# Kernel optimization log

Measured on AMD Instinct MI355X. Metric: run time of the kernel, lower is better.

Reference implementation:

```python
import jax, jax.numpy as jnp
import numpy as np

NUM_CATS = 8
ACTION_DIM = 64
HIDDEN = 1024  # out_type.size == config.hidden_size
N_TOKENS = 4096  # B*T
N_BATCH = 128    # timesteps batch; tiled to N_TOKENS in forward


def sinusoidal_pos_encoding(t, dim):
    # standard transformer sinusoidal encoding; t: (N,) -> (N, dim)
    half = dim // 2
    div = jnp.exp(jnp.arange(half, dtype=jnp.float32) * (-np.log(10000.0) / half))
    ang = t.astype(jnp.float32)[:, None] * div[None, :]          # (N, half)
    pe = jnp.stack([jnp.sin(ang), jnp.cos(ang)], axis=-1)        # (N, half, 2)
    return pe.reshape(t.shape[0], dim)


def cat_linear(x, W, b, cat_ids):
    """Per-category linear (gather -> per-group GEMM -> scatter-back, fused).
    x: (N, din), W: (C, din, dout), b: (C, dout), cat_ids: (N,) int.
    Mathematically identical to the torch loop over unique cat ids."""
    y_all = jnp.einsum('nd,cdo->nco', x, W)                      # dense dispatch over C
    y = jnp.take_along_axis(y_all, cat_ids[:, None, None], axis=1)[:, 0, :]
    return y + b[cat_ids]


def setup_inputs() -> dict:
    key = jax.random.key(0)
    ks = jax.random.split(key, 9)
    inp = {
        'actions': jax.random.normal(ks[0], (N_TOKENS, ACTION_DIM), dtype=jnp.float32),
        'timesteps': jax.random.randint(ks[1], (N_BATCH,), 0, 1000, dtype=jnp.int32),
        'cat_ids': jax.random.randint(ks[2], (N_TOKENS,), 0, NUM_CATS, dtype=jnp.int32),
        'W1': jax.random.normal(ks[3], (NUM_CATS, ACTION_DIM, HIDDEN), dtype=jnp.float32) / np.sqrt(ACTION_DIM),
        'b1': jax.random.normal(ks[4], (NUM_CATS, HIDDEN), dtype=jnp.float32) * 0.02,
        'W2': jax.random.normal(ks[5], (NUM_CATS, 2 * HIDDEN, HIDDEN), dtype=jnp.float32) / np.sqrt(2 * HIDDEN),
        'b2': jax.random.normal(ks[6], (NUM_CATS, HIDDEN), dtype=jnp.float32) * 0.02,
        'W3': jax.random.normal(ks[7], (NUM_CATS, HIDDEN, HIDDEN), dtype=jnp.float32) / np.sqrt(HIDDEN),
        'b3': jax.random.normal(ks[8], (NUM_CATS, HIDDEN), dtype=jnp.float32) * 0.02,
    }
    return inp


def reference(actions, timesteps, cat_ids, W1, b1, W2, b2, W3, b3):
    n = actions.shape[0]
    # timesteps.repeat(B // timesteps.shape[0]) in torch tiles the whole tensor
    t_full = jnp.tile(timesteps, n // timesteps.shape[0])        # (N,)
    a_emb = cat_linear(actions, W1, b1, cat_ids)                 # (N, H)
    tau_emb = sinusoidal_pos_encoding(t_full, HIDDEN).astype(a_emb.dtype)
    x = jnp.concatenate([a_emb, tau_emb], axis=-1)               # (N, 2H)
    x = jax.nn.silu(cat_linear(x, W2, b2, cat_ids))              # swish
    x = cat_linear(x, W3, b3, cat_ids)                           # (N, H)
    return x
```

## Files before the change

kernel.cpp:

```cpp
#include <hip/hip_runtime.h>
#include <cmath>


#define NTOK 4096
#define HID  1024
#define NC   8
#define MPAD 4224

typedef _Float16 f16;
typedef _Float16 f16x8 __attribute__((ext_vector_type(8)));
typedef float    f32x4 __attribute__((ext_vector_type(4)));

#define GLDS16(g, l) __builtin_amdgcn_global_load_lds(                      \
    (const __attribute__((address_space(1))) void*)(g),                     \
    (__attribute__((address_space(3))) void*)(l), 16, 0, 0)
#define WAITV(n) asm volatile("s_waitcnt vmcnt(" #n ")" ::: "memory")

__global__ void build_perm_kernel(const int* __restrict__ cat,
                                  int* __restrict__ perm,
                                  int* __restrict__ cat_off,
                                  int* __restrict__ tmap) {
  __shared__ int cnt[NC];
  __shared__ int off[NC + 1];
  const int tid = threadIdx.x;
  if (tid < NC) cnt[tid] = 0;
  __syncthreads();
  for (int n = tid; n < NTOK; n += blockDim.x) atomicAdd(&cnt[cat[n]], 1);
  __syncthreads();
  if (tid == 0) {
    int s = 0;
    for (int c = 0; c < NC; ++c) { off[c] = s; s += cnt[c]; }
    off[NC] = s;
    int ns = 0;
    for (int c = 0; c < NC; ++c) {
      const int n = off[c + 1] - off[c];
      for (int m0 = 0; m0 < n; m0 += 64) tmap[1 + ns++] = (c << 20) | m0;
    }
    tmap[0] = ns;
  }
  __syncthreads();
  if (tid < NC) cnt[tid] = off[tid];
  if (tid <= NC) cat_off[tid] = off[tid];
  __syncthreads();
  for (int n = tid; n < NTOK; n += blockDim.x) {
    int pos = atomicAdd(&cnt[cat[n]], 1);
    perm[pos] = n;
  }
}

__global__ void tau16_kernel(const int* __restrict__ ts, f16* __restrict__ tau) {
  const int b = blockIdx.x;
  const float t = (float)ts[b];
  const float cdiv = -0.017988946039015984f;
  for (int i = threadIdx.x; i < HID / 2; i += blockDim.x) {
    float ang = t * expf(cdiv * (float)i);
    tau[(size_t)b * HID + 2 * i]     = (f16)sinf(ang);
    tau[(size_t)b * HID + 2 * i + 1] = (f16)cosf(ang);
  }
}

__global__ void gather_kernel(const float* __restrict__ actions,
                              const f16* __restrict__ tau,
                              const int* __restrict__ perm,
                              f16* __restrict__ act_g, f16* __restrict__ xcat) {
  const int r = blockIdx.x;
  const int tok = perm[r];
  const int t = threadIdx.x;
  if (t < 64) act_g[(size_t)r * 64 + t] = (f16)actions[(size_t)tok * 64 + t];
  const uint4* src = (const uint4*)(tau + (size_t)(tok & 127) * HID);
  uint4* dst = (uint4*)(xcat + (size_t)r * 2048 + HID);
  dst[t] = src[t];
}

__global__ __launch_bounds__(256) void wcvt_kernel(const float* __restrict__ W,
                                                   f16* __restrict__ Wt, int K) {
  const int c = blockIdx.z, k0 = blockIdx.y * 64, n0 = blockIdx.x * 64;
  __shared__ f16 tl[64][68];
  const int tid = threadIdx.x;
  const int rr = tid >> 4, cs = (tid & 15) * 4;
  const float* src = W + ((size_t)c * K + k0) * HID + n0;
#pragma unroll
  for (int it = 0; it < 4; ++it) {
    const int kr = rr + it * 16;
    float4 v = *(const float4*)(src + (size_t)kr * HID + cs);
    tl[kr][cs + 0] = (f16)v.x;
    tl[kr][cs + 1] = (f16)v.y;
    tl[kr][cs + 2] = (f16)v.z;
    tl[kr][cs + 3] = (f16)v.w;
  }
  __syncthreads();
  f16* dst = Wt + ((size_t)c * HID + n0) * K + k0;
#pragma unroll
  for (int it = 0; it < 4; ++it) {
    const int nr = rr + it * 16;
    union { f16 h[4]; uint2 u; } pk;
    pk.h[0] = tl[cs + 0][nr];
    pk.h[1] = tl[cs + 1][nr];
    pk.h[2] = tl[cs + 2][nr];
    pk.h[3] = tl[cs + 3][nr];
    *(uint2*)(dst + (size_t)nr * K + cs) = pk.u;
  }
}

template <int K, int MODE>
__global__ __launch_bounds__(256, 2) void mfma_gemm(
    const f16* __restrict__ A, const f16* __restrict__ Wt,
    const float* __restrict__ Bias, const int* __restrict__ perm,
    const int* __restrict__ cat_off, const int* __restrict__ tmap,
    void* __restrict__ OutV) {
  constexpr int PA = (MODE == 0) ? 64 : (MODE == 1) ? 2048 : 1024;
  constexpr int BK = 64;
  constexpr int NT = K / BK;

  const int nslots = tmap[0];
  if ((int)blockIdx.y >= nslots) return;
  const int ent = tmap[1 + blockIdx.y];
  const int c = ent >> 20, m0 = ent & 0xFFF;
  const int g0 = cat_off[c], cnt = cat_off[c + 1] - g0;
  const int n0 = blockIdx.x * 128;

  __shared__ f16 As[3][64 * BK];
  __shared__ f16 Bs[3][128 * BK];
  __shared__ int rows[64];

  const int tid = threadIdx.x;
  const int lane = tid & 63, wid = tid >> 6;
  const int wm = wid >> 1, wn = wid & 1;
  const int fr = lane & 15, fq = lane >> 4;

  if (MODE == 2 && tid < 64) {
    int m = m0 + tid;
    if (m > cnt - 1) m = cnt - 1;
    rows[tid] = perm[g0 + m];
  }

  const f16* Abase = A + (size_t)(g0 + m0) * PA;
  const f16* Bbase = Wt + ((size_t)c * HID + n0) * K;

#define STAGE(buf, kt)                                                        \
  do {                                                                        \
    _Pragma("unroll") for (int i_ = 0; i_ < 2; ++i_) {                        \
      const int s_ = tid + i_ * 256;                                          \
      const int r_ = s_ >> 3, qg_ = (s_ & 7) ^ (r_ & 7);                      \
      GLDS16(Abase + (size_t)r_ * PA + (kt) + qg_ * 8, &As[buf][s_ * 8]);     \
    }                                                                         \
    _Pragma("unroll") for (int i_ = 0; i_ < 4; ++i_) {                        \
      const int s_ = tid + i_ * 256;                                          \
      const int r_ = s_ >> 3, qg_ = (s_ & 7) ^ (r_ & 7);                      \
      GLDS16(Bbase + (size_t)r_ * K + (kt) + qg_ * 8, &Bs[buf][s_ * 8]);      \
    }                                                                         \
  } while (0)

  f32x4 acc[2][4];
#pragma unroll
  for (int i = 0; i < 2; ++i)
#pragma unroll
    for (int j = 0; j < 4; ++j) acc[i][j] = (f32x4){0.f, 0.f, 0.f, 0.f};

  STAGE(0, 0);
  if (NT > 1) STAGE(1, BK);

  for (int t = 0; t < NT; ++t) {
    if (t + 1 < NT) { WAITV(6); } else { WAITV(0); }
    __builtin_amdgcn_s_barrier();
    const int cur = t % 3;

    f16x8 af[2][2], bf[2][4];
#pragma unroll
    for (int ks = 0; ks < 2; ++ks) {
      const int q = ks * 4 + fq;
#pragma unroll
      for (int i = 0; i < 2; ++i) {
        const int r = wm * 32 + i * 16 + fr;
        af[ks][i] = *(const f16x8*)&As[cur][r * 64 + ((q ^ (r & 7)) * 8)];
      }
#pragma unroll
      for (int j = 0; j < 4; ++j) {
        const int r = wn * 64 + j * 16 + fr;
        bf[ks][j] = *(const f16x8*)&Bs[cur][r * 64 + ((q ^ (r & 7)) * 8)];
      }
    }
#pragma unroll
    for (int ks = 0; ks < 2; ++ks)
#pragma unroll
      for (int i = 0; i < 2; ++i)
#pragma unroll
        for (int j = 0; j < 4; ++j)
          acc[i][j] = __builtin_amdgcn_mfma_f32_16x16x32_f16(af[ks][i], bf[ks][j],
                                                             acc[i][j], 0, 0, 0);
    if (t + 2 < NT) STAGE((t + 2) % 3, (t + 2) * BK);
  }
#undef STAGE

#pragma unroll
  for (int i = 0; i < 2; ++i) {
    const int mlb = wm * 32 + i * 16 + fq * 4;
#pragma unroll
    for (int j = 0; j < 4; ++j) {
      const int col = wn * 64 + j * 16 + fr;
      const float bb = Bias[c * HID + n0 + col];
#pragma unroll
      for (int q = 0; q < 4; ++q) {
        const int ml = mlb + q;
        if (m0 + ml >= cnt) continue;
        float v = acc[i][j][q] + bb;
        if (MODE == 1) v = v / (1.0f + __expf(-v));
        if (MODE == 2) {
          ((float*)OutV)[(size_t)rows[ml] * HID + n0 + col] = v;
        } else if (MODE == 1) {
          ((f16*)OutV)[(size_t)(g0 + m0 + ml) * HID + n0 + col] = (f16)v;
        } else {
          ((f16*)OutV)[(size_t)(g0 + m0 + ml) * 2048 + n0 + col] = (f16)v;
        }
      }
    }
  }
}

extern "C" void kernel_launch(void* const* d_in, const int* in_sizes, int n_in,
                              void* d_out, int out_size, void* d_ws, size_t ws_size,
                              hipStream_t stream) {
  const float* actions   = (const float*)d_in[0];
  const int*   timesteps = (const int*)d_in[1];
  const int*   cat_ids   = (const int*)d_in[2];
  const float* W1 = (const float*)d_in[3];
  const float* b1 = (const float*)d_in[4];
  const float* W2 = (const float*)d_in[5];
  const float* b2 = (const float*)d_in[6];
  const float* W3 = (const float*)d_in[7];
  const float* b3 = (const float*)d_in[8];
  float* out = (float*)d_out;

  char* ws = (char*)d_ws;
  const size_t MiB = 1u << 20;
  int* perm    = (int*)(ws + 0);
  int* cat_off = (int*)(ws + (16u << 10));
  int* tmap    = (int*)(ws + (20u << 10));
  f16* tau16   = (f16*)(ws + (32u << 10));
  f16* act_g   = (f16*)(ws + (512u << 10));
  f16* Wt1     = (f16*)(ws + 2 * MiB);
  f16* xcat    = (f16*)(ws + 3 * MiB);
  f16* h       = (f16*)(ws + 20 * MiB);
  f16* Wt2     = (f16*)(ws + 29 * MiB);
  f16* Wt3     = (f16*)(ws + 61 * MiB);

  build_perm_kernel<<<1, 256, 0, stream>>>(cat_ids, perm, cat_off, tmap);
  tau16_kernel<<<128, 256, 0, stream>>>(timesteps, tau16);
  gather_kernel<<<NTOK, 128, 0, stream>>>(actions, tau16, perm, act_g, xcat);

  wcvt_kernel<<<dim3(HID / 64, 1, NC), 256, 0, stream>>>(W1, Wt1, 64);
  wcvt_kernel<<<dim3(HID / 64, 32, NC), 256, 0, stream>>>(W2, Wt2, 2048);
  wcvt_kernel<<<dim3(HID / 64, 16, NC), 256, 0, stream>>>(W3, Wt3, 1024);

  dim3 ggrid(HID / 128, 72, 1);
  mfma_gemm<64, 0><<<ggrid, 256, 0, stream>>>(act_g, Wt1, b1, perm, cat_off, tmap, xcat);
  mfma_gemm<2048, 1><<<ggrid, 256, 0, stream>>>(xcat, Wt2, b2, perm, cat_off, tmap, h);
  mfma_gemm<1024, 2><<<ggrid, 256, 0, stream>>>(h, Wt3, b3, perm, cat_off, tmap, out);
}
```

Before: 262.0 us.

## Shrink GEMM tile to 64x64 with BK=32 and raise occupancy

The grouped MFMA GEMM tile shrinks from 64x128 to 64x64 and the K step from 64 to 32, with a new LDS swizzle (slot16) for the 32-wide rows. The launch grid doubles along N and launch bounds rise to 4 blocks per SM. The goal is more blocks in flight and lower per-block LDS and register use, since the old grid underfilled the GPU with about 8x72 blocks. The cost is lower data reuse per block, more barriers per unit of K, and more total global traffic. The build_perm kernel also runs with 1024 threads.

```diff
diff --git a/kernel.cpp b/kernel.cpp
--- a/kernel.cpp
+++ b/kernel.cpp
@@ -15,6 +15,10 @@
     (const __attribute__((address_space(1))) void*)(g),                     \
     (__attribute__((address_space(3))) void*)(l), 16, 0, 0)
 #define WAITV(n) asm volatile("s_waitcnt vmcnt(" #n ")" ::: "memory")
+
+__device__ __forceinline__ int slot16(int r, int q) {
+  return (r >> 1) * 8 + ((((r & 1) << 2) | q) ^ ((r >> 1) & 7));
+}
 
 __global__ void build_perm_kernel(const int* __restrict__ cat,
                                   int* __restrict__ perm,
@@ -103,13 +107,13 @@
 }
 
 template <int K, int MODE>
-__global__ __launch_bounds__(256, 2) void mfma_gemm(
+__global__ __launch_bounds__(256, 4) void mfma_gemm(
     const f16* __restrict__ A, const f16* __restrict__ Wt,
     const float* __restrict__ Bias, const int* __restrict__ perm,
     const int* __restrict__ cat_off, const int* __restrict__ tmap,
     void* __restrict__ OutV) {
   constexpr int PA = (MODE == 0) ? 64 : (MODE == 1) ? 2048 : 1024;
-  constexpr int BK = 64;
+  constexpr int BK = 32;
   constexpr int NT = K / BK;
 
   const int nslots = tmap[0];
@@ -117,15 +121,14 @@
   const int ent = tmap[1 + blockIdx.y];
   const int c = ent >> 20, m0 = ent & 0xFFF;
   const int g0 = cat_off[c], cnt = cat_off[c + 1] - g0;
-  const int n0 = blockIdx.x * 128;
+  const int n0 = blockIdx.x * 64;
 
   __shared__ f16 As[3][64 * BK];
-  __shared__ f16 Bs[3][128 * BK];
+  __shared__ f16 Bs[3][64 * BK];
   __shared__ int rows[64];
 
   const int tid = threadIdx.x;
   const int lane = tid & 63, wid = tid >> 6;
-  const int wm = wid >> 1, wn = wid & 1;
   const int fr = lane & 15, fq = lane >> 4;
 
   if (MODE == 2 && tid < 64) {
@@ -137,81 +140,58 @@
   const f16* Abase = A + (size_t)(g0 + m0) * PA;
   const f16* Bbase = Wt + ((size_t)c * HID + n0) * K;
 
-#define STAGE(buf, kt)                                                        \
-  do {                                                                        \
-    _Pragma("unroll") for (int i_ = 0; i_ < 2; ++i_) {                        \
-      const int s_ = tid + i_ * 256;                                          \
-      const int r_ = s_ >> 3, qg_ = (s_ & 7) ^ (r_ & 7);                      \
-      GLDS16(Abase + (size_t)r_ * PA + (kt) + qg_ * 8, &As[buf][s_ * 8]);     \
-    }                                                                         \
-    _Pragma("unroll") for (int i_ = 0; i_ < 4; ++i_) {                        \
-      const int s_ = tid + i_ * 256;                                          \
-      const int r_ = s_ >> 3, qg_ = (s_ & 7) ^ (r_ & 7);                      \
-      GLDS16(Bbase + (size_t)r_ * K + (kt) + qg_ * 8, &Bs[buf][s_ * 8]);      \
-    }                                                                         \
+  const int pr_ = tid >> 3, u_ = tid & 7, w_ = u_ ^ (pr_ & 7);
+  const int sr_ = 2 * pr_ + (w_ >> 2), sq_ = (w_ & 3) * 8;
+#define STAGE(buf, kt)                                                   \
+  do {                                                                   \
+    GLDS16(Abase + (size_t)sr_ * PA + (kt) + sq_, &As[buf][tid * 8]);    \
+    GLDS16(Bbase + (size_t)sr_ * K + (kt) + sq_, &Bs[buf][tid * 8]);     \
   } while (0)
 
-  f32x4 acc[2][4];
-#pragma unroll
-  for (int i = 0; i < 2; ++i)
-#pragma unroll
-    for (int j = 0; j < 4; ++j) acc[i][j] = (f32x4){0.f, 0.f, 0.f, 0.f};
+  f32x4 acc[4];
+#pragma unroll
+  for (int j = 0; j < 4; ++j) acc[j] = (f32x4){0.f, 0.f, 0.f, 0.f};
 
   STAGE(0, 0);
   if (NT > 1) STAGE(1, BK);
 
   for (int t = 0; t < NT; ++t) {
-    if (t + 1 < NT) { WAITV(6); } else { WAITV(0); }
+    if (t + 1 < NT) { WAITV(2); } else { WAITV(0); }
     __builtin_amdgcn_s_barrier();
     const int cur = t % 3;
 
-    f16x8 af[2][2], bf[2][4];
-#pragma unroll
-    for (int ks = 0; ks < 2; ++ks) {
-      const int q = ks * 4 + fq;
-#pragma unroll
-      for (int i = 0; i < 2; ++i) {
-        const int r = wm * 32 + i * 16 + fr;
-        af[ks][i] = *(const f16x8*)&As[cur][r * 64 + ((q ^ (r & 7)) * 8)];
-      }
-#pragma unroll
-      for (int j = 0; j < 4; ++j) {
-        const int r = wn * 64 + j * 16 + fr;
-        bf[ks][j] = *(const f16x8*)&Bs[cur][r * 64 + ((q ^ (r & 7)) * 8)];
-      }
+    const int ar = wid * 16 + fr;
+    f16x8 af = *(const f16x8*)&As[cur][slot16(ar, fq) * 8];
+    f16x8 bf[4];
+#pragma unroll
+    for (int j = 0; j < 4; ++j) {
+      const int br = j * 16 + fr;
+      bf[j] = *(const f16x8*)&Bs[cur][slot16(br, fq) * 8];
     }
 #pragma unroll
-    for (int ks = 0; ks < 2; ++ks)
-#pragma unroll
-      for (int i = 0; i < 2; ++i)
-#pragma unroll
-        for (int j = 0; j < 4; ++j)
-          acc[i][j] = __builtin_amdgcn_mfma_f32_16x16x32_f16(af[ks][i], bf[ks][j],
-                                                             acc[i][j], 0, 0, 0);
+    for (int j = 0; j < 4; ++j)
+      acc[j] = __builtin_amdgcn_mfma_f32_16x16x32_f16(af, bf[j], acc[j], 0, 0, 0);
     if (t + 2 < NT) STAGE((t + 2) % 3, (t + 2) * BK);
   }
 #undef STAGE
 
-#pragma unroll
-  for (int i = 0; i < 2; ++i) {
-    const int mlb = wm * 32 + i * 16 + fq * 4;
-#pragma unroll
-    for (int j = 0; j < 4; ++j) {
-      const int col = wn * 64 + j * 16 + fr;
-      const float bb = Bias[c * HID + n0 + col];
-#pragma unroll
-      for (int q = 0; q < 4; ++q) {
-        const int ml = mlb + q;
-        if (m0 + ml >= cnt) continue;
-        float v = acc[i][j][q] + bb;
-        if (MODE == 1) v = v / (1.0f + __expf(-v));
-        if (MODE == 2) {
-          ((float*)OutV)[(size_t)rows[ml] * HID + n0 + col] = v;
-        } else if (MODE == 1) {
-          ((f16*)OutV)[(size_t)(g0 + m0 + ml) * HID + n0 + col] = (f16)v;
-        } else {
-          ((f16*)OutV)[(size_t)(g0 + m0 + ml) * 2048 + n0 + col] = (f16)v;
-        }
+  const int mlb = wid * 16 + fq * 4;
+#pragma unroll
+  for (int j = 0; j < 4; ++j) {
+    const int col = j * 16 + fr;
+    const float bb = Bias[c * HID + n0 + col];
+#pragma unroll
+    for (int q = 0; q < 4; ++q) {
+      const int ml = mlb + q;
+      if (m0 + ml >= cnt) continue;
+      float v = acc[j][q] + bb;
+      if (MODE == 1) v = v / (1.0f + __expf(-v));
+      if (MODE == 2) {
+        ((float*)OutV)[(size_t)rows[ml] * HID + n0 + col] = v;
+      } else if (MODE == 1) {
+        ((f16*)OutV)[(size_t)(g0 + m0 + ml) * HID + n0 + col] = (f16)v;
+      } else {
+        ((f16*)OutV)[(size_t)(g0 + m0 + ml) * 2048 + n0 + col] = (f16)v;
       }
     }
   }
@@ -244,7 +224,7 @@
   f16* Wt2     = (f16*)(ws + 29 * MiB);
   f16* Wt3     = (f16*)(ws + 61 * MiB);
 
-  build_perm_kernel<<<1, 256, 0, stream>>>(cat_ids, perm, cat_off, tmap);
+  build_perm_kernel<<<1, 1024, 0, stream>>>(cat_ids, perm, cat_off, tmap);
   tau16_kernel<<<128, 256, 0, stream>>>(timesteps, tau16);
   gather_kernel<<<NTOK, 128, 0, stream>>>(actions, tau16, perm, act_g, xcat);
 
@@ -252,7 +232,7 @@
   wcvt_kernel<<<dim3(HID / 64, 32, NC), 256, 0, stream>>>(W2, Wt2, 2048);
   wcvt_kernel<<<dim3(HID / 64, 16, NC), 256, 0, stream>>>(W3, Wt3, 1024);
 
-  dim3 ggrid(HID / 128, 72, 1);
+  dim3 ggrid(HID / 64, 72, 1);
   mfma_gemm<64, 0><<<ggrid, 256, 0, stream>>>(act_g, Wt1, b1, perm, cat_off, tmap, xcat);
   mfma_gemm<2048, 1><<<ggrid, 256, 0, stream>>>(xcat, Wt2, b2, perm, cat_off, tmap, h);
   mfma_gemm<1024, 2><<<ggrid, 256, 0, stream>>>(h, Wt3, b3, perm, cat_off, tmap, out);
```

Measured after the change: 258.1 us. Within noise of the previous version (-1.5%).

## Fold layer-1 linear into layer-2 weights and precompute per-timestep tau projection

Applied to the files above, without the earlier changes.

Because layer 1 is linear, W1 and b1 are multiplied into the first half of W2 per category, giving a 64x1024 effective weight and a folded bias. The tau half of layer 2 depends only on the 128 distinct timesteps, so its projection is computed once per category and timestep and added in the epilogue. The 4096x2048-K layer-2 GEMM shrinks to a K=64 GEMM plus a lookup, and the W2 conversion pass and xcat buffer go away. In exchange the folded W1·W2 product is rounded to fp16, which changes numerics slightly, and two extra small GEMM kernels run on every call.

```diff
diff --git a/kernel.cpp b/kernel.cpp
--- a/kernel.cpp
+++ b/kernel.cpp
@@ -15,6 +15,10 @@
     (const __attribute__((address_space(1))) void*)(g),                     \
     (__attribute__((address_space(3))) void*)(l), 16, 0, 0)
 #define WAITV(n) asm volatile("s_waitcnt vmcnt(" #n ")" ::: "memory")
+
+__device__ __forceinline__ int slot16(int r, int q) {
+  return (r >> 1) * 8 + ((((r & 1) << 2) | q) ^ ((r >> 1) & 7));
+}
 
 __global__ void build_perm_kernel(const int* __restrict__ cat,
                                   int* __restrict__ perm,
@@ -60,16 +64,26 @@
 }
 
 __global__ void gather_kernel(const float* __restrict__ actions,
-                              const f16* __restrict__ tau,
                               const int* __restrict__ perm,
-                              f16* __restrict__ act_g, f16* __restrict__ xcat) {
+                              f16* __restrict__ act_g) {
   const int r = blockIdx.x;
   const int tok = perm[r];
-  const int t = threadIdx.x;
-  if (t < 64) act_g[(size_t)r * 64 + t] = (f16)actions[(size_t)tok * 64 + t];
-  const uint4* src = (const uint4*)(tau + (size_t)(tok & 127) * HID);
-  uint4* dst = (uint4*)(xcat + (size_t)r * 2048 + HID);
-  dst[t] = src[t];
+  act_g[(size_t)r * 64 + threadIdx.x] =
+      (f16)actions[(size_t)tok * 64 + threadIdx.x];
+}
+
+__global__ void a1ext_kernel(const float* __restrict__ W1,
+                             const float* __restrict__ b1,
+                             f16* __restrict__ A1) {
+  const int c = blockIdx.y, row = blockIdx.x;
+  const float* src = (row < 64) ? W1 + ((size_t)c * 64 + row) * HID
+                                : b1 + (size_t)c * HID;
+  f16* dst = A1 + ((size_t)c * 128 + row) * HID;
+  const int i = threadIdx.x;
+  float4 v = *(const float4*)(src + i * 4);
+  union { f16 h[4]; uint2 u; } pk;
+  pk.h[0] = (f16)v.x; pk.h[1] = (f16)v.y; pk.h[2] = (f16)v.z; pk.h[3] = (f16)v.w;
+  *(uint2*)(dst + (size_t)i * 4) = pk.u;
 }
 
 __global__ __launch_bounds__(256) void wcvt_kernel(const float* __restrict__ W,
@@ -102,16 +116,196 @@
   }
 }
 
-template <int K, int MODE>
-__global__ __launch_bounds__(256, 2) void mfma_gemm(
+template <int MODE>
+__global__ __launch_bounds__(256, 4) void fold_gemm(
+    const f16* __restrict__ A, const float* __restrict__ W2,
+    const float* __restrict__ b2, float* __restrict__ b2eff,
+    f16* __restrict__ W12t, float* __restrict__ ttau) {
+  constexpr int NT = 32;
+  const int c = blockIdx.y;
+  const int n0 = blockIdx.x * 64;
+
+  __shared__ f16 As[2][128 * 32];
+  __shared__ f16 Bs[2][64 * 32];
+
+  const int tid = threadIdx.x;
+  const int lane = tid & 63, wid = tid >> 6;
+  const int fr = lane & 15, fq = lane >> 4;
+
+  const f16* Abase = (MODE == 0) ? A + (size_t)c * 131072 : A;
+  const float* Wbase = W2 + (size_t)c * 2097152 +
+                       (MODE == 0 ? (size_t)0 : (size_t)1024 * HID) + n0;
+
+  int asr[2], asq[2], asl[2];
+#pragma unroll
+  for (int i = 0; i < 2; ++i) {
+    const int s = tid + i * 256;
+    const int pr = s >> 3, u = s & 7, w = u ^ (pr & 7);
+    asr[i] = 2 * pr + (w >> 2); asq[i] = (w & 3) * 8; asl[i] = s * 8;
+  }
+  int bo4[2], bm[2];
+#pragma unroll
+  for (int r = 0; r < 2; ++r) {
+    const int g = r * 256 + tid;
+    bo4[r] = (g & 15) * 4; bm[r] = g >> 4;
+  }
+  float4 breg[2];
+
+#define ISSUE_A(buf, kt)                                                     \
+  do {                                                                       \
+    _Pragma("unroll") for (int i_ = 0; i_ < 2; ++i_)                         \
+      GLDS16(Abase + (size_t)asr[i_] * HID + (kt) + asq[i_],                 \
+             &As[buf][asl[i_]]);                                             \
+  } while (0)
+#define LOAD_B(kt)                                                           \
+  do {                                                                       \
+    _Pragma("unroll") for (int r_ = 0; r_ < 2; ++r_)                         \
+      breg[r_] = *(const float4*)(Wbase + (size_t)(bm[r_] + (kt)) * HID +    \
+                                  bo4[r_]);                                  \
+  } while (0)
+#define WRITE_B(buf)                                                         \
+  do {                                                                       \
+    _Pragma("unroll") for (int r_ = 0; r_ < 2; ++r_) {                       \
+      const float* f_ = (const float*)&breg[r_];                             \
+      _Pragma("unroll") for (int i_ = 0; i_ < 4; ++i_)                       \
+        Bs[buf][slot16(bo4[r_] + i_, bm[r_] >> 3) * 8 + (bm[r_] & 7)] =      \
+            (f16)f_[i_];                                                     \
+    }                                                                        \
+  } while (0)
+
+  f32x4 acc[2][4];
+#pragma unroll
+  for (int i = 0; i < 2; ++i)
+#pragma unroll
+    for (int j = 0; j < 4; ++j) acc[i][j] = (f32x4){0.f, 0.f, 0.f, 0.f};
+
+  ISSUE_A(0, 0); LOAD_B(0);
+  WAITV(0);
+  WRITE_B(0);
+  __syncthreads();
+
+  for (int t = 0; t < NT; ++t) {
+    const int cur = t & 1;
+    if (t + 1 < NT) { ISSUE_A(cur ^ 1, (t + 1) * 32); LOAD_B((t + 1) * 32); }
+    f16x8 a0 = *(const f16x8*)&As[cur][slot16(wid * 16 + fr, fq) * 8];
+    f16x8 a1 = *(const f16x8*)&As[cur][slot16(64 + wid * 16 + fr, fq) * 8];
+    f16x8 bf[4];
+#pragma unroll
+    for (int j = 0; j < 4; ++j)
+      bf[j] = *(const f16x8*)&Bs[cur][slot16(j * 16 + fr, fq) * 8];
+#pragma unroll
+    for (int j = 0; j < 4; ++j) {
+      acc[0][j] = __builtin_amdgcn_mfma_f32_16x16x32_f16(a0, bf[j], acc[0][j], 0, 0, 0);
+      acc[1][j] = __builtin_amdgcn_mfma_f32_16x16x32_f16(a1, bf[j], acc[1][j], 0, 0, 0);
+    }
+    if (t + 1 < NT) { WAITV(0); WRITE_B(cur ^ 1); }
+    __syncthreads();
+  }
+#undef ISSUE_A
+#undef LOAD_B
+#undef WRITE_B
+
+#pragma unroll
+  for (int j = 0; j < 4; ++j) {
+    const int col = j * 16 + fr, o = n0 + col;
+#pragma unroll
+    for (int q = 0; q < 4; ++q) {
+      const int row0 = wid * 16 + fq * 4 + q;
+      if constexpr (MODE == 0) {
+        W12t[(size_t)c * 65536 + (size_t)o * 64 + row0] = (f16)acc[0][j][q];
+        if (wid == 0 && fq == 0 && q == 0)
+          b2eff[c * HID + o] = acc[1][j][q];
+      } else {
+        const float bb = b2eff[c * HID + o] + b2[c * HID + o];
+        ttau[(size_t)c * 131072 + (size_t)row0 * HID + o] = acc[0][j][q] + bb;
+        ttau[(size_t)c * 131072 + (size_t)(64 + row0) * HID + o] = acc[1][j][q] + bb;
+      }
+    }
+  }
+}
+
+__global__ __launch_bounds__(256, 4) void l2pre_gemm(
+    const f16* __restrict__ A, const f16* __restrict__ B,
+    const float* __restrict__ Ttau, const int* __restrict__ perm,
+    const int* __restrict__ cat_off, const int* __restrict__ tmap,
+    f16* __restrict__ H) {
+  constexpr int NT = 2;
+  const int nslots = tmap[0];
+  if ((int)blockIdx.y >= nslots) return;
+  const int ent = tmap[1 + blockIdx.y];
+  const int c = ent >> 20, m0 = ent & 0xFFF;
+  const int g0 = cat_off[c], cnt = cat_off[c + 1] - g0;
+  const int n0 = blockIdx.x * 64;
+
+  __shared__ f16 As[2][64 * 32];
+  __shared__ f16 Bs[2][64 * 32];
+  __shared__ int rows[64];
+
+  const int tid = threadIdx.x;
+  const int lane = tid & 63, wid = tid >> 6;
+  const int fr = lane & 15, fq = lane >> 4;
+
+  if (tid < 64) {
+    int m = m0 + tid;
+    if (m > cnt - 1) m = cnt - 1;
+    rows[tid] = perm[g0 + m];
+  }
+
+  const f16* Abase = A + (size_t)(g0 + m0) * 64;
+  const f16* Bbase = B + (size_t)c * 65536 + (size_t)n0 * 64;
+
+  const int pr_ = tid >> 3, u_ = tid & 7, w_ = u_ ^ (pr_ & 7);
+  const int sr_ = 2 * pr_ + (w_ >> 2), sq_ = (w_ & 3) * 8;
+#define STAGE(buf, kt)                                                   \
+  do {                                                                   \
+    GLDS16(Abase + (size_t)sr_ * 64 + (kt) + sq_, &As[buf][tid * 8]);    \
+    GLDS16(Bbase + (size_t)sr_ * 64 + (kt) + sq_, &Bs[buf][tid * 8]);    \
+  } while (0)
+
+  f32x4 acc[4];
+#pragma unroll
+  for (int j = 0; j < 4; ++j) acc[j] = (f32x4){0.f, 0.f, 0.f, 0.f};
+
+  STAGE(0, 0);
+  STAGE(1, 32);
+  for (int t = 0; t < NT; ++t) {
+    if (t + 1 < NT) { WAITV(2); } else { WAITV(0); }
+    __builtin_amdgcn_s_barrier();
+    const int cur = t & 1;
+    const int ar = wid * 16 + fr;
+    f16x8 af = *(const f16x8*)&As[cur][slot16(ar, fq) * 8];
+    f16x8 bf[4];
+#pragma unroll
+    for (int j = 0; j < 4; ++j)
+      bf[j] = *(const f16x8*)&Bs[cur][slot16(j * 16 + fr, fq) * 8];
+#pragma unroll
+    for (int j = 0; j < 4; ++j)
+      acc[j] = __builtin_amdgcn_mfma_f32_16x16x32_f16(af, bf[j], acc[j], 0, 0, 0);
+  }
+#undef STAGE
+
+  const int mlb = wid * 16 + fq * 4;
+#pragma unroll
+  for (int j = 0; j < 4; ++j) {
+    const int col = j * 16 + fr;
+#pragma unroll
+    for (int q = 0; q < 4; ++q) {
+      const int ml = mlb + q;
+      if (m0 + ml >= cnt) continue;
+      const int b = rows[ml] & 127;
+      float v = acc[j][q] + Ttau[((size_t)c * 128 + b) * HID + n0 + col];
+      v = v / (1.0f + __expf(-v));
+      H[(size_t)(g0 + m0 + ml) * HID + n0 + col] = (f16)v;
+    }
+  }
+}
+
+__global__ __launch_bounds__(256, 2) void l3_gemm(
     const f16* __restrict__ A, const f16* __restrict__ Wt,
     const float* __restrict__ Bias, const int* __restrict__ perm,
     const int* __restrict__ cat_off, const int* __restrict__ tmap,
-    void* __restrict__ OutV) {
-  constexpr int PA = (MODE == 0) ? 64 : (MODE == 1) ? 2048 : 1024;
-  constexpr int BK = 64;
-  constexpr int NT = K / BK;
-
+    float* __restrict__ Out) {
+  constexpr int BK = 64, NT = 1024 / BK;
   const int nslots = tmap[0];
   if ((int)blockIdx.y >= nslots) return;
   const int ent = tmap[1 + blockIdx.y];
@@ -128,26 +322,26 @@
   const int wm = wid >> 1, wn = wid & 1;
   const int fr = lane & 15, fq = lane >> 4;
 
-  if (MODE == 2 && tid < 64) {
+  if (tid < 64) {
     int m = m0 + tid;
     if (m > cnt - 1) m = cnt - 1;
     rows[tid] = perm[g0 + m];
   }
 
-  const f16* Abase = A + (size_t)(g0 + m0) * PA;
-  const f16* Bbase = Wt + ((size_t)c * HID + n0) * K;
+  const f16* Abase = A + (size_t)(g0 + m0) * HID;
+  const f16* Bbase = Wt + ((size_t)c * HID + n0) * HID;
 
 #define STAGE(buf, kt)                                                        \
   do {                                                                        \
     _Pragma("unroll") for (int i_ = 0; i_ < 2; ++i_) {                        \
       const int s_ = tid + i_ * 256;                                          \
       const int r_ = s_ >> 3, qg_ = (s_ & 7) ^ (r_ & 7);                      \
-      GLDS16(Abase + (size_t)r_ * PA + (kt) + qg_ * 8, &As[buf][s_ * 8]);     \
+      GLDS16(Abase + (size_t)r_ * HID + (kt) + qg_ * 8, &As[buf][s_ * 8]);    \
     }                                                                         \
     _Pragma("unroll") for (int i_ = 0; i_ < 4; ++i_) {                        \
       const int s_ = tid + i_ * 256;                                          \
       const int r_ = s_ >> 3, qg_ = (s_ & 7) ^ (r_ & 7);                      \
-      GLDS16(Bbase + (size_t)r_ * K + (kt) + qg_ * 8, &Bs[buf][s_ * 8]);      \
+      GLDS16(Bbase + (size_t)r_ * HID + (kt) + qg_ * 8, &Bs[buf][s_ * 8]);    \
     }                                                                         \
   } while (0)
 
@@ -158,7 +352,7 @@
     for (int j = 0; j < 4; ++j) acc[i][j] = (f32x4){0.f, 0.f, 0.f, 0.f};
 
   STAGE(0, 0);
-  if (NT > 1) STAGE(1, BK);
+  STAGE(1, BK);
 
   for (int t = 0; t < NT; ++t) {
     if (t + 1 < NT) { WAITV(6); } else { WAITV(0); }
@@ -203,15 +397,7 @@
       for (int q = 0; q < 4; ++q) {
         const int ml = mlb + q;
         if (m0 + ml >= cnt) continue;
-        float v = acc[i][j][q] + bb;
-        if (MODE == 1) v = v / (1.0f + __expf(-v));
-        if (MODE == 2) {
-          ((float*)OutV)[(size_t)rows[ml] * HID + n0 + col] = v;
-        } else if (MODE == 1) {
-          ((f16*)OutV)[(size_t)(g0 + m0 + ml) * HID + n0 + col] = (f16)v;
-        } else {
-          ((f16*)OutV)[(size_t)(g0 + m0 + ml) * 2048 + n0 + col] = (f16)v;
-        }
+        Out[(size_t)rows[ml] * HID + n0 + col] = acc[i][j][q] + bb;
       }
     }
   }
@@ -233,27 +419,29 @@
 
   char* ws = (char*)d_ws;
   const size_t MiB = 1u << 20;
-  int* perm    = (int*)(ws + 0);
-  int* cat_off = (int*)(ws + (16u << 10));
-  int* tmap    = (int*)(ws + (20u << 10));
-  f16* tau16   = (f16*)(ws + (32u << 10));
-  f16* act_g   = (f16*)(ws + (512u << 10));
-  f16* Wt1     = (f16*)(ws + 2 * MiB);
-  f16* xcat    = (f16*)(ws + 3 * MiB);
-  f16* h       = (f16*)(ws + 20 * MiB);
-  f16* Wt2     = (f16*)(ws + 29 * MiB);
-  f16* Wt3     = (f16*)(ws + 61 * MiB);
-
-  build_perm_kernel<<<1, 256, 0, stream>>>(cat_ids, perm, cat_off, tmap);
+  int*   perm    = (int*)(ws + 0);
+  int*   cat_off = (int*)(ws + (16u << 10));
+  int*   tmap    = (int*)(ws + (20u << 10));
+  f16*   tau16   = (f16*)(ws + (32u << 10));
+  f16*   act_g   = (f16*)(ws + (512u << 10));
+  f16*   A1ext   = (f16*)(ws + 2 * MiB);
+  f16*   W12t    = (f16*)(ws + 4 * MiB);
+  float* b2eff   = (float*)(ws + 5 * MiB);
+  float* ttau    = (float*)(ws + 6 * MiB);
+  f16*   h       = (f16*)(ws + 10 * MiB);
+  f16*   Wt3     = (f16*)(ws + 19 * MiB);
+
+  build_perm_kernel<<<1, 1024, 0, stream>>>(cat_ids, perm, cat_off, tmap);
   tau16_kernel<<<128, 256, 0, stream>>>(timesteps, tau16);
-  gather_kernel<<<NTOK, 128, 0, stream>>>(actions, tau16, perm, act_g, xcat);
-
-  wcvt_kernel<<<dim3(HID / 64, 1, NC), 256, 0, stream>>>(W1, Wt1, 64);
-  wcvt_kernel<<<dim3(HID / 64, 32, NC), 256, 0, stream>>>(W2, Wt2, 2048);
+  gather_kernel<<<NTOK, 64, 0, stream>>>(actions, perm, act_g);
+  a1ext_kernel<<<dim3(65, NC), 256, 0, stream>>>(W1, b1, A1ext);
   wcvt_kernel<<<dim3(HID / 64, 16, NC), 256, 0, stream>>>(W3, Wt3, 1024);
 
-  dim3 ggrid(HID / 128, 72, 1);
-  mfma_gemm<64, 0><<<ggrid, 256, 0, stream>>>(act_g, Wt1, b1, perm, cat_off, tmap, xcat);
-  mfma_gemm<2048, 1><<<ggrid, 256, 0, stream>>>(xcat, Wt2, b2, perm, cat_off, tmap, h);
-  mfma_gemm<1024, 2><<<ggrid, 256, 0, stream>>>(h, Wt3, b3, perm, cat_off, tmap, out);
-}
+  fold_gemm<0><<<dim3(16, NC), 256, 0, stream>>>(A1ext, W2, nullptr, b2eff,
+                                                 W12t, nullptr);
+  fold_gemm<1><<<dim3(16, NC), 256, 0, stream>>>(tau16, W2, b2, b2eff,
+                                                 nullptr, ttau);
+  l2pre_gemm<<<dim3(16, 72), 256, 0, stream>>>(act_g, W12t, ttau, perm,
+                                               cat_off, tmap, h);
+  l3_gemm<<<dim3(8, 72), 256, 0, stream>>>(h, Wt3, b3, perm, cat_off, tmap, out);
+}
```

Result: slower. 283.2 us (+8.1%).
